# Kernel optimization log

Hardware: AMD Instinct MI355X
Metric: run time of the kernel (lower is better)

The kernel has to match this reference:

```python
import jax, jax.numpy as jnp
import numpy as np

L = 2          # num_layers
B = 32         # batch
T = 64         # max_sequence_length (= source len here)
H = 1024       # hidden_size
E = 1024       # embedding_size (== H so layer weights stack uniformly)
V = 16000      # vocab (in == out)


def _cell(x, h, c, Wih, Whh, bih, bhh):
    # PyTorch LSTM gate order: i, f, g, o
    g = x @ Wih.T + h @ Whh.T + (bih + bhh)
    i, f, gg, o = jnp.split(g, 4, axis=-1)
    c_new = jax.nn.sigmoid(f) * c + jax.nn.sigmoid(i) * jnp.tanh(gg)
    h_new = jax.nn.sigmoid(o) * jnp.tanh(c_new)
    return h_new, c_new


def _stack_step(h, c, x, Wih, Whh, bih, bhh):
    # h, c: (L, B, H); x: (B, E). Fixed small loop over layers.
    hs, cs, inp = [], [], x
    for l in range(L):
        nh, nc = _cell(inp, h[l], c[l], Wih[l], Whh[l], bih[l], bhh[l])
        hs.append(nh); cs.append(nc); inp = nh
    return jnp.stack(hs), jnp.stack(cs), inp


def setup_inputs() -> dict:
    key = jax.random.key(0)
    ks = jax.random.split(key, 16)
    s = 1.0 / np.sqrt(H)
    U = lambda k, shp: jax.random.uniform(k, shp, jnp.float32, -s, s)
    inp = {
        "input_ids": jax.random.randint(ks[0], (B, T), 0, V),
        "output_ids": jax.random.randint(ks[1], (B, T), 0, V),
        "enc_emb": jax.random.normal(ks[2], (V, E), jnp.float32),
        "enc_Wih": U(ks[3], (L, 4 * H, H)),
        "enc_Whh": U(ks[4], (L, 4 * H, H)),
        "enc_bih": U(ks[5], (L, 4 * H)),
        "enc_bhh": U(ks[6], (L, 4 * H)),
        "dec_emb": jax.random.normal(ks[7], (V, E), jnp.float32),
        "dec_Wih": U(ks[8], (L, 4 * H, H)),
        "dec_Whh": U(ks[9], (L, 4 * H, H)),
        "dec_bih": U(ks[10], (L, 4 * H)),
        "dec_bhh": U(ks[11], (L, 4 * H)),
        "Wout": U(ks[12], (V, H)),
        "bout": U(ks[13], (V,)),
    }
    return inp


def reference(input_ids, output_ids, enc_emb, enc_Wih, enc_Whh, enc_bih, enc_bhh,
              dec_emb, dec_Wih, dec_Whh, dec_bih, dec_bhh, Wout, bout):
    dtype = enc_emb.dtype
    # ---- Encoder: run LSTM over source, keep final (h, c) ----
    enc_x = enc_emb[input_ids]                      # (B, T, E); dropout is identity (eval)
    h0 = jnp.zeros((L, B, H), dtype)
    c0 = jnp.zeros((L, B, H), dtype)

    def enc_step(carry, xt):
        h, c = carry
        h, c, _ = _stack_step(h, c, xt, enc_Wih, enc_Whh, enc_bih, enc_bhh)
        return (h, c), None

    (h, c), _ = jax.lax.scan(enc_step, (h0, c0), jnp.swapaxes(enc_x, 0, 1))

    # ---- Decoder: teacher-forced; step i consumes output_ids[:, i-1] ----
    dec_x = dec_emb[output_ids[:, : T - 1]]         # (B, T-1, E)

    def dec_step(carry, xt):
        h, c = carry
        h, c, top = _stack_step(h, c, xt, dec_Wih, dec_Whh, dec_bih, dec_bhh)
        logit = top @ Wout.T + bout                  # (B, V)
        return (h, c), logit

    (_, _), logits_seq = jax.lax.scan(dec_step, (h, c), jnp.swapaxes(dec_x, 0, 1))

    # ---- Assemble logits like the torch code ----
    logits = jnp.zeros((B, T, V), dtype)
    # torch: logits[:, 0, output_ids[:, 0]] = 1  (broadcasts over both batch dims)
    logits = logits.at[:, 0, output_ids[:, 0]].set(1.0)
    logits = logits.at[:, 1:, :].set(jnp.swapaxes(logits_seq, 0, 1))
    return logits
```

## Files before the change

### kernel.cpp

```cpp
#include <hip/hip_runtime.h>

namespace {

constexpr int kB = 32;
constexpr int kT = 64;
constexpr int kH = 1024;
constexpr int kE = 1024;
constexpr int kV = 16000;
constexpr int kG = 4096;

typedef __attribute__((ext_vector_type(8))) short short8v;
typedef __attribute__((ext_vector_type(4))) float f32x4;

__device__ __forceinline__ float sigmoid_f(float x) {
  return 1.0f / (1.0f + __expf(-x));
}
__device__ __forceinline__ unsigned short f2bf(float x) {
  unsigned int u = __builtin_bit_cast(unsigned int, x);
  u = (u + 0x7FFFu + ((u >> 16) & 1u)) >> 16;
  return (unsigned short)u;
}
__device__ __forceinline__ float bf2f(unsigned short h) {
  return __builtin_bit_cast(float, (unsigned int)h << 16);
}

__global__ void zero_t0_kernel(float* __restrict__ out) {
  int idx = blockIdx.x * blockDim.x + threadIdx.x;
  if (idx >= kB * kV) return;
  int b = idx / kV, v = idx % kV;
  __builtin_nontemporal_store(0.0f, &out[(size_t)b * kT * kV + v]);
}

__global__ void ones_t0_kernel(const int* __restrict__ output_ids,
                               float* __restrict__ out) {
  int b = threadIdx.x >> 5;
  int j = threadIdx.x & 31;
  int id = output_ids[j * kT];
  out[(size_t)b * kT * kV + id] = 1.0f;
}

__global__ __launch_bounds__(256)
void convert_frag(const float* __restrict__ src, unsigned short* __restrict__ dst,
                  int nchunks) {
  const int idx = blockIdx.x * 256 + threadIdx.x;
  if (idx >= nchunks) return;
  const int lane = idx & 63;
  const int s = (idx >> 6) & 31;
  const int rg = idx >> 11;
  const int row = rg * 16 + (lane & 15);
  const int k = s * 32 + ((lane >> 4) << 3);
  const float4* p = reinterpret_cast<const float4*>(src + (size_t)row * kH + k);
  float4 v0 = p[0], v1 = p[1];
  short8v o;
  o[0] = (short)f2bf(v0.x); o[1] = (short)f2bf(v0.y);
  o[2] = (short)f2bf(v0.z); o[3] = (short)f2bf(v0.w);
  o[4] = (short)f2bf(v1.x); o[5] = (short)f2bf(v1.y);
  o[6] = (short)f2bf(v1.z); o[7] = (short)f2bf(v1.w);
  *reinterpret_cast<short8v*>(dst + (size_t)idx * 8) = o;
}

__global__ __launch_bounds__(256)
void convert_cell(const float* __restrict__ src, unsigned short* __restrict__ dst,
                  int nchunks) {
  const int idx = blockIdx.x * 256 + threadIdx.x;
  if (idx >= nchunks) return;
  const int l = idx & 63;
  const int kstep = (idx >> 6) & 31;
  const int uq = (idx >> 11) & 1;
  const int ub = idx >> 12;
  const int n = l & 15;
  const int row = (n >> 2) * kH + ub * 8 + uq * 4 + (n & 3);
  const int k = kstep * 32 + ((l >> 4) << 3);
  const float4* p = reinterpret_cast<const float4*>(src + (size_t)row * kH + k);
  float4 v0 = p[0], v1 = p[1];
  short8v o;
  o[0] = (short)f2bf(v0.x); o[1] = (short)f2bf(v0.y);
  o[2] = (short)f2bf(v0.z); o[3] = (short)f2bf(v0.w);
  o[4] = (short)f2bf(v1.x); o[5] = (short)f2bf(v1.y);
  o[6] = (short)f2bf(v1.z); o[7] = (short)f2bf(v1.w);
  *reinterpret_cast<short8v*>(dst + (size_t)idx * 8) = o;
}

__global__ __launch_bounds__(256)
void gather_frag(const float* __restrict__ emb, const int* __restrict__ ids,
                 unsigned short* __restrict__ dst, int ntiles) {
  const int idx = blockIdx.x * 256 + threadIdx.x;
  const int lane = idx & 63;
  const int s = (idx >> 6) & 31;
  const int tile = idx >> 11;
  if (tile >= ntiles) return;
  const int m = tile * 16 + (lane & 15);
  const int t = m >> 5, b = m & 31;
  const int id = ids[b * kT + t];
  const int k = s * 32 + ((lane >> 4) << 3);
  const float4* p = reinterpret_cast<const float4*>(emb + (size_t)id * kE + k);
  float4 v0 = p[0], v1 = p[1];
  short8v o;
  o[0] = (short)f2bf(v0.x); o[1] = (short)f2bf(v0.y);
  o[2] = (short)f2bf(v0.z); o[3] = (short)f2bf(v0.w);
  o[4] = (short)f2bf(v1.x); o[5] = (short)f2bf(v1.y);
  o[6] = (short)f2bf(v1.z); o[7] = (short)f2bf(v1.w);
  *reinterpret_cast<short8v*>(dst + (size_t)idx * 8) = o;
}

__global__ __launch_bounds__(256)
void proj_mfma(const unsigned short* __restrict__ Af,
               const unsigned short* __restrict__ Bf,
               const float* __restrict__ b0, const float* __restrict__ b1,
               unsigned short* __restrict__ dst, int nmt) {
  const int w = threadIdx.x >> 6, lane = threadIdx.x & 63;
  const int mg = blockIdx.x, ng = blockIdx.y;
  f32x4 acc[4][2] = {};
  const unsigned short* Ab[4];
  const unsigned short* Bb[2];
#pragma unroll
  for (int i = 0; i < 4; ++i) {
    int tile = mg * 4 + i;
    if (tile > nmt - 1) tile = nmt - 1;
    Ab[i] = Af + (size_t)tile * 16384 + lane * 8;
  }
#pragma unroll
  for (int j = 0; j < 2; ++j) {
    const int nt = ng * 8 + w * 2 + j;
    Bb[j] = Bf + (size_t)nt * 16384 + lane * 8;
  }
#pragma unroll 2
  for (int s = 0; s < 32; ++s) {
    short8v a[4], b[2];
#pragma unroll
    for (int i = 0; i < 4; ++i) a[i] = *reinterpret_cast<const short8v*>(Ab[i] + s * 512);
#pragma unroll
    for (int j = 0; j < 2; ++j) b[j] = *reinterpret_cast<const short8v*>(Bb[j] + s * 512);
#pragma unroll
    for (int i = 0; i < 4; ++i)
#pragma unroll
      for (int j = 0; j < 2; ++j)
        acc[i][j] = __builtin_amdgcn_mfma_f32_16x16x32_bf16(a[i], b[j], acc[i][j], 0, 0, 0);
  }
#pragma unroll
  for (int i = 0; i < 4; ++i) {
    const int tile = mg * 4 + i;
    if (tile >= nmt) continue;
    const int mbase = tile * 16 + ((lane >> 4) << 2);
#pragma unroll
    for (int j = 0; j < 2; ++j) {
      const int n = (ng * 8 + w * 2 + j) * 16 + (lane & 15);
      const float bj = b0[n] + b1[n];
      const int g = n >> 10;
      const int u = n & 1023;
      const int q = u >> 2;
      const int uu = u & 3;
#pragma unroll
      for (int r = 0; r < 4; ++r) {
        const int m2 = mbase + r;
        const int t = m2 >> 5, mb = m2 & 31;
        dst[(size_t)t * kB * kG + (size_t)(q * 32 + mb) * 16 + g * 4 + uu] =
            f2bf(acc[i][j][r] + bj);
      }
    }
  }
}

__global__ __launch_bounds__(256)
void out_gemm_mfma(const unsigned short* __restrict__ Af,
                   const unsigned short* __restrict__ Bf,
                   const float* __restrict__ bias, float* __restrict__ out) {
  const int w = threadIdx.x >> 6, lane = threadIdx.x & 63;
  const int mg = blockIdx.x, ng = blockIdx.y;
  __shared__ float LsF[64 * 260];
  f32x4 acc[4][4] = {};
  const unsigned short* Ab[4];
  const unsigned short* Bb[4];
#pragma unroll
  for (int i = 0; i < 4; ++i) {
    int tile = mg * 4 + i;
    if (tile > 125) tile = 125;
    Ab[i] = Af + (size_t)tile * 16384 + lane * 8;
  }
#pragma unroll
  for (int j = 0; j < 4; ++j) {
    int nt = ng * 16 + w * 4 + j;
    if (nt > 999) nt = 999;
    Bb[j] = Bf + (size_t)nt * 16384 + lane * 8;
  }
#pragma unroll 2
  for (int s = 0; s < 32; ++s) {
    short8v a[4], b[4];
#pragma unroll
    for (int i = 0; i < 4; ++i) a[i] = *reinterpret_cast<const short8v*>(Ab[i] + s * 512);
#pragma unroll
    for (int j = 0; j < 4; ++j) b[j] = *reinterpret_cast<const short8v*>(Bb[j] + s * 512);
#pragma unroll
    for (int i = 0; i < 4; ++i)
#pragma unroll
      for (int j = 0; j < 4; ++j)
        acc[i][j] = __builtin_amdgcn_mfma_f32_16x16x32_bf16(a[i], b[j], acc[i][j], 0, 0, 0);
  }
#pragma unroll
  for (int i = 0; i < 4; ++i) {
    const int r2b = i * 16 + ((lane >> 4) << 2);
#pragma unroll
    for (int j = 0; j < 4; ++j) {
      const int nloc = (w * 4 + j) * 16 + (lane & 15);
#pragma unroll
      for (int r = 0; r < 4; ++r) LsF[(r2b + r) * 260 + nloc] = acc[i][j][r];
    }
  }
  __syncthreads();
  const int nglob = ng * 256 + lane * 4;
  if (nglob >= kV) return;
  const f32x4 b4 = *reinterpret_cast<const f32x4*>(&bias[nglob]);
#pragma unroll
  for (int it = 0; it < 16; ++it) {
    const int r2 = w * 16 + it;
    const int m = mg * 64 + r2;
    if (m >= 2016) break;
    f32x4 v = *reinterpret_cast<const f32x4*>(&LsF[r2 * 260 + lane * 4]);
    v += b4;
    const int sd = m >> 5, bb = m & 31;
    f32x4* dst = reinterpret_cast<f32x4*>(
        &out[(size_t)bb * kT * kV + (size_t)(sd + 1) * kV + nglob]);
    __builtin_nontemporal_store(v, dst);
  }
}

struct CellJob {
  const unsigned short* A0;
  const unsigned short* A1;
  const unsigned short* Wih1;
  const unsigned short* Whh1;
  const unsigned short* Whh0;
  const unsigned short* xprojc;
  const float* bih1;
  const float* bhh1;
  float* c0;
  float* c1;
  unsigned short* h0_out;
  unsigned short* h1_out;
  unsigned short* htop_out;
  int has_l0, has_l1;
};

__global__ __launch_bounds__(512)
void lstm_pair(CellJob J) {
  const int q = blockIdx.x;
  const int tid = threadIdx.x;
  const int wave = tid >> 6;
  const int lane = tid & 63;
  __shared__ alignas(16) float Ls[3][8][2][64][4];

  f32x4 aI0 = {0.f, 0.f, 0.f, 0.f}, aI1 = {0.f, 0.f, 0.f, 0.f};
  f32x4 aJ0 = {0.f, 0.f, 0.f, 0.f}, aJ1 = {0.f, 0.f, 0.f, 0.f};
  f32x4 aH0 = {0.f, 0.f, 0.f, 0.f}, aH1 = {0.f, 0.f, 0.f, 0.f};
  const int ksb = wave * 4;
#pragma unroll
  for (int s = 0; s < 4; ++s) {
    const int ks = ksb + s;
    const size_t widx = ((size_t)(q * 32 + ks) * 64 + lane) * 8;
    const short8v a00 =
        *reinterpret_cast<const short8v*>(J.A0 + (size_t)(ks * 64 + lane) * 8);
    const short8v a01 =
        *reinterpret_cast<const short8v*>(J.A0 + (size_t)((32 + ks) * 64 + lane) * 8);
    if (J.has_l1) {
      const short8v bi = *reinterpret_cast<const short8v*>(J.Wih1 + widx);
      aI0 = __builtin_amdgcn_mfma_f32_16x16x32_bf16(a00, bi, aI0, 0, 0, 0);
      aI1 = __builtin_amdgcn_mfma_f32_16x16x32_bf16(a01, bi, aI1, 0, 0, 0);
      const short8v a10 =
          *reinterpret_cast<const short8v*>(J.A1 + (size_t)(ks * 64 + lane) * 8);
      const short8v a11 =
          *reinterpret_cast<const short8v*>(J.A1 + (size_t)((32 + ks) * 64 + lane) * 8);
      const short8v bh1 = *reinterpret_cast<const short8v*>(J.Whh1 + widx);
      aJ0 = __builtin_amdgcn_mfma_f32_16x16x32_bf16(a10, bh1, aJ0, 0, 0, 0);
      aJ1 = __builtin_amdgcn_mfma_f32_16x16x32_bf16(a11, bh1, aJ1, 0, 0, 0);
    }
    if (J.has_l0) {
      const short8v bh0 = *reinterpret_cast<const short8v*>(J.Whh0 + widx);
      aH0 = __builtin_amdgcn_mfma_f32_16x16x32_bf16(a00, bh0, aH0, 0, 0, 0);
      aH1 = __builtin_amdgcn_mfma_f32_16x16x32_bf16(a01, bh0, aH1, 0, 0, 0);
    }
  }
  *reinterpret_cast<f32x4*>(&Ls[0][wave][0][lane][0]) = aI0;
  *reinterpret_cast<f32x4*>(&Ls[0][wave][1][lane][0]) = aI1;
  *reinterpret_cast<f32x4*>(&Ls[1][wave][0][lane][0]) = aJ0;
  *reinterpret_cast<f32x4*>(&Ls[1][wave][1][lane][0]) = aJ1;
  *reinterpret_cast<f32x4*>(&Ls[2][wave][0][lane][0]) = aH0;
  *reinterpret_cast<f32x4*>(&Ls[2][wave][1][lane][0]) = aH1;
  __syncthreads();

  if (tid < 128) {
    const int m = tid >> 2;
    const int ul = tid & 3;
    const int u = q * 4 + ul;
    const int mt = m >> 4, r = m & 3;
    const int lm = (m & 12) << 2;
    const int ksu = u >> 5;
    const int lane3 = (m & 15) | (((u >> 3) & 3) << 4);
    const int e = u & 7;
    const size_t fidx = (size_t)((mt * 32 + ksu) * 64 + lane3) * 8 + e;

    if (J.has_l0) {
      float g0[4];
#pragma unroll
      for (int g = 0; g < 4; ++g) {
        const int ln = (g * 4 + ul) | lm;
        float v = 0.f;
#pragma unroll
        for (int ww = 0; ww < 8; ++ww) v += Ls[2][ww][mt][ln][r];
        v += bf2f(J.xprojc[(q * 32 + m) * 16 + g * 4 + ul]);
        g0[g] = v;
      }
      const float cold = J.c0[m * kH + u];
      const float cnew = sigmoid_f(g0[1]) * cold + sigmoid_f(g0[0]) * tanhf(g0[2]);
      const float hnew = sigmoid_f(g0[3]) * tanhf(cnew);
      J.c0[m * kH + u] = cnew;
      J.h0_out[fidx] = f2bf(hnew);
    }
    if (J.has_l1) {
      float g1[4];
#pragma unroll
      for (int g = 0; g < 4; ++g) {
        const int ln = (g * 4 + ul) | lm;
        float v = 0.f;
#pragma unroll
        for (int ww = 0; ww < 8; ++ww)
          v += Ls[0][ww][mt][ln][r] + Ls[1][ww][mt][ln][r];
        v += J.bih1[g * kH + u] + J.bhh1[g * kH + u];
        g1[g] = v;
      }
      const float cold = J.c1[m * kH + u];
      const float cnew = sigmoid_f(g1[1]) * cold + sigmoid_f(g1[0]) * tanhf(g1[2]);
      const float hnew = sigmoid_f(g1[3]) * tanhf(cnew);
      J.c1[m * kH + u] = cnew;
      const unsigned short hb = f2bf(hnew);
      J.h1_out[fidx] = hb;
      if (J.htop_out) J.htop_out[fidx] = hb;
    }
  }
}

}

extern "C" void kernel_launch(void* const* d_in, const int* in_sizes, int n_in,
                              void* d_out, int out_size, void* d_ws, size_t ws_size,
                              hipStream_t stream) {
  const int* input_ids = (const int*)d_in[0];
  const int* output_ids = (const int*)d_in[1];
  const float* enc_emb = (const float*)d_in[2];
  const float* enc_Wih = (const float*)d_in[3];
  const float* enc_Whh = (const float*)d_in[4];
  const float* enc_bih = (const float*)d_in[5];
  const float* enc_bhh = (const float*)d_in[6];
  const float* dec_emb = (const float*)d_in[7];
  const float* dec_Wih = (const float*)d_in[8];
  const float* dec_Whh = (const float*)d_in[9];
  const float* dec_bih = (const float*)d_in[10];
  const float* dec_bhh = (const float*)d_in[11];
  const float* Wout = (const float*)d_in[12];
  const float* bout = (const float*)d_in[13];
  float* out = (float*)d_out;
  char* ws = (char*)d_ws;

  const size_t WL = (size_t)kG * kH;

  size_t off = 0;
  unsigned short* wout_frag = (unsigned short*)(ws + 0);
  unsigned short* xproj_enc = (unsigned short*)(ws + off); off += (size_t)kT * kB * kG * 2;
  unsigned short* xin_enc = (unsigned short*)(ws + off); off += (size_t)kT * kB * kH * 2;
  unsigned short* wih0_enc = (unsigned short*)(ws + off); off += WL * 2;
  unsigned short* wih0_dec = (unsigned short*)(ws + off); off += WL * 2;
  unsigned short* xproj_dec = (unsigned short*)(ws + off); off += (size_t)(kT - 1) * kB * kG * 2;
  unsigned short* xin_dec = (unsigned short*)(ws + off); off += (size_t)(kT - 1) * kB * kH * 2;
  unsigned short* htop_frag = xin_dec;
  float* c0 = (float*)(ws + off); off += (size_t)kB * kH * 4;
  float* c1 = (float*)(ws + off); off += (size_t)kB * kH * 4;
  unsigned short* h0swz[2];
  unsigned short* h1swz[2];
  h0swz[0] = (unsigned short*)(ws + off); off += (size_t)kB * kH * 2;
  h0swz[1] = (unsigned short*)(ws + off); off += (size_t)kB * kH * 2;
  h1swz[0] = (unsigned short*)(ws + off); off += (size_t)kB * kH * 2;
  h1swz[1] = (unsigned short*)(ws + off); off += (size_t)kB * kH * 2;
  unsigned short* wswz[6];
  for (int i = 0; i < 6; ++i) { wswz[i] = (unsigned short*)(ws + off); off += WL * 2; }

  (void)hipMemsetAsync(c0, 0, (size_t)kB * kH * (4 + 4 + 2 + 2 + 2 + 2), stream);

  const int wchunks = kG * (kH / 8);
  convert_cell<<<2048, 256, 0, stream>>>(enc_Whh, wswz[0], wchunks);
  convert_cell<<<2048, 256, 0, stream>>>(enc_Wih + WL, wswz[1], wchunks);
  convert_cell<<<2048, 256, 0, stream>>>(enc_Whh + WL, wswz[2], wchunks);
  convert_cell<<<2048, 256, 0, stream>>>(dec_Whh, wswz[3], wchunks);
  convert_cell<<<2048, 256, 0, stream>>>(dec_Wih + WL, wswz[4], wchunks);
  convert_cell<<<2048, 256, 0, stream>>>(dec_Whh + WL, wswz[5], wchunks);
  convert_frag<<<2048, 256, 0, stream>>>(enc_Wih, wih0_enc, wchunks);
  convert_frag<<<2048, 256, 0, stream>>>(dec_Wih, wih0_dec, wchunks);

  gather_frag<<<128 * 8, 256, 0, stream>>>(enc_emb, input_ids, xin_enc, 128);
  gather_frag<<<126 * 8, 256, 0, stream>>>(dec_emb, output_ids, xin_dec, 126);

  proj_mfma<<<dim3(32, 32), 256, 0, stream>>>(xin_enc, wih0_enc, enc_bih, enc_bhh,
                                              xproj_enc, 128);
  proj_mfma<<<dim3(32, 32), 256, 0, stream>>>(xin_dec, wih0_dec, dec_bih, dec_bhh,
                                              xproj_dec, 126);

  for (int p = 0; p <= 127; ++p) {
    CellJob J = {};
    J.has_l0 = (p <= 126);
    J.has_l1 = (p >= 1);
    J.A0 = h0swz[p & 1];
    J.A1 = h1swz[(p + 1) & 1];
    J.c0 = c0;
    J.c1 = c1;
    if (J.has_l0) {
      J.Whh0 = (p < kT) ? wswz[0] : wswz[3];
      J.xprojc = (p < kT) ? (xproj_enc + (size_t)p * kB * kG)
                          : (xproj_dec + (size_t)(p - kT) * kB * kG);
      J.h0_out = h0swz[(p + 1) & 1];
    } else {
      J.Whh0 = wswz[3];
      J.xprojc = xproj_dec;
      J.h0_out = h0swz[(p + 1) & 1];
    }
    if (J.has_l1) {
      const bool e1 = (p - 1) < kT;
      J.Wih1 = e1 ? wswz[1] : wswz[4];
      J.Whh1 = e1 ? wswz[2] : wswz[5];
      J.bih1 = (e1 ? enc_bih : dec_bih) + kG;
      J.bhh1 = (e1 ? enc_bhh : dec_bhh) + kG;
      J.h1_out = h1swz[p & 1];
      J.htop_out = (p - 1 >= kT) ? (htop_frag + (size_t)(p - 1 - kT) * kB * kH)
                                 : nullptr;
    } else {
      J.Wih1 = wswz[1];
      J.Whh1 = wswz[2];
      J.bih1 = enc_bih + kG;
      J.bhh1 = enc_bhh + kG;
      J.h1_out = h1swz[p & 1];
      J.htop_out = nullptr;
    }
    lstm_pair<<<256, 512, 0, stream>>>(J);
    if (p == 63) {
      convert_frag<<<8000, 256, 0, stream>>>(Wout, wout_frag, kV * (kH / 8));
    }
  }

  zero_t0_kernel<<<(kB * kV + 255) / 256, 256, 0, stream>>>(out);
  ones_t0_kernel<<<1, kB * kB, 0, stream>>>(output_ids, out);

  out_gemm_mfma<<<dim3(32, 63), 256, 0, stream>>>(htop_frag, wout_frag, bout, out);
}
```

Before: 1.174 ms.

## Process two gate tiles per LSTM block and swizzle output GEMM blocks

The recurrent lstm_pair kernel now has each block compute two unit groups, so each loaded activation fragment is reused across twice as many weight tiles, and the grid drops from 256 to 128 blocks. The layer guards around the MFMA loop are removed, so both layers' products are always computed. The output GEMM maps a 1D grid through an XCD-style swizzle for better L2 locality, and it writes its epilogue through a half-sized LDS buffer in two phases to lower shared-memory use. The trade-off is that the per-step recurrent kernel now uses only half as many CUs, which may hurt a latency-bound step.

```diff
diff --git a/kernel.cpp b/kernel.cpp
--- a/kernel.cpp
+++ b/kernel.cpp
@@ -166,8 +166,10 @@
                    const unsigned short* __restrict__ Bf,
                    const float* __restrict__ bias, float* __restrict__ out) {
   const int w = threadIdx.x >> 6, lane = threadIdx.x & 63;
-  const int mg = blockIdx.x, ng = blockIdx.y;
-  __shared__ float LsF[64 * 260];
+  const int bid = blockIdx.x;
+  const int swz = (bid & 7) * 252 + (bid >> 3);
+  const int mg = swz & 31, ng = swz >> 5;
+  __shared__ float LsF[32 * 260];
   f32x4 acc[4][4] = {};
   const unsigned short* Ab[4];
   const unsigned short* Bb[4];
@@ -196,31 +198,38 @@
       for (int j = 0; j < 4; ++j)
         acc[i][j] = __builtin_amdgcn_mfma_f32_16x16x32_bf16(a[i], b[j], acc[i][j], 0, 0, 0);
   }
-#pragma unroll
-  for (int i = 0; i < 4; ++i) {
-    const int r2b = i * 16 + ((lane >> 4) << 2);
-#pragma unroll
-    for (int j = 0; j < 4; ++j) {
-      const int nloc = (w * 4 + j) * 16 + (lane & 15);
-#pragma unroll
-      for (int r = 0; r < 4; ++r) LsF[(r2b + r) * 260 + nloc] = acc[i][j][r];
-    }
-  }
-  __syncthreads();
   const int nglob = ng * 256 + lane * 4;
-  if (nglob >= kV) return;
-  const f32x4 b4 = *reinterpret_cast<const f32x4*>(&bias[nglob]);
-#pragma unroll
-  for (int it = 0; it < 16; ++it) {
-    const int r2 = w * 16 + it;
-    const int m = mg * 64 + r2;
-    if (m >= 2016) break;
-    f32x4 v = *reinterpret_cast<const f32x4*>(&LsF[r2 * 260 + lane * 4]);
-    v += b4;
-    const int sd = m >> 5, bb = m & 31;
-    f32x4* dst = reinterpret_cast<f32x4*>(
-        &out[(size_t)bb * kT * kV + (size_t)(sd + 1) * kV + nglob]);
-    __builtin_nontemporal_store(v, dst);
+  f32x4 b4 = {0.f, 0.f, 0.f, 0.f};
+  if (nglob < kV) b4 = *reinterpret_cast<const f32x4*>(&bias[nglob]);
+#pragma unroll
+  for (int ph = 0; ph < 2; ++ph) {
+    if (ph) __syncthreads();
+#pragma unroll
+    for (int i2 = 0; i2 < 2; ++i2) {
+      const int i = ph * 2 + i2;
+      const int r2b = i2 * 16 + ((lane >> 4) << 2);
+#pragma unroll
+      for (int j = 0; j < 4; ++j) {
+        const int nloc = (w * 4 + j) * 16 + (lane & 15);
+#pragma unroll
+        for (int r = 0; r < 4; ++r) LsF[(r2b + r) * 260 + nloc] = acc[i][j][r];
+      }
+    }
+    __syncthreads();
+    if (nglob < kV) {
+#pragma unroll
+      for (int it = 0; it < 8; ++it) {
+        const int r2l = w * 8 + it;
+        const int m = mg * 64 + ph * 32 + r2l;
+        if (m >= 2016) break;
+        f32x4 v = *reinterpret_cast<const f32x4*>(&LsF[r2l * 260 + lane * 4]);
+        v += b4;
+        const int sd = m >> 5, bb = m & 31;
+        f32x4* dst = reinterpret_cast<f32x4*>(
+            &out[(size_t)bb * kT * kV + (size_t)(sd + 1) * kV + nglob]);
+        __builtin_nontemporal_store(v, dst);
+      }
+    }
   }
 }
 
@@ -243,53 +252,58 @@
 
 __global__ __launch_bounds__(512)
 void lstm_pair(CellJob J) {
-  const int q = blockIdx.x;
+  const int blk = blockIdx.x;
   const int tid = threadIdx.x;
   const int wave = tid >> 6;
   const int lane = tid & 63;
-  __shared__ alignas(16) float Ls[3][8][2][64][4];
-
-  f32x4 aI0 = {0.f, 0.f, 0.f, 0.f}, aI1 = {0.f, 0.f, 0.f, 0.f};
-  f32x4 aJ0 = {0.f, 0.f, 0.f, 0.f}, aJ1 = {0.f, 0.f, 0.f, 0.f};
-  f32x4 aH0 = {0.f, 0.f, 0.f, 0.f}, aH1 = {0.f, 0.f, 0.f, 0.f};
+  __shared__ alignas(16) float Ls[2][3][8][2][64][4];
+
+  f32x4 aI[2][2] = {};
+  f32x4 aJ[2][2] = {};
+  f32x4 aH[2][2] = {};
   const int ksb = wave * 4;
 #pragma unroll
   for (int s = 0; s < 4; ++s) {
     const int ks = ksb + s;
-    const size_t widx = ((size_t)(q * 32 + ks) * 64 + lane) * 8;
     const short8v a00 =
         *reinterpret_cast<const short8v*>(J.A0 + (size_t)(ks * 64 + lane) * 8);
     const short8v a01 =
         *reinterpret_cast<const short8v*>(J.A0 + (size_t)((32 + ks) * 64 + lane) * 8);
-    if (J.has_l1) {
+    const short8v a10 =
+        *reinterpret_cast<const short8v*>(J.A1 + (size_t)(ks * 64 + lane) * 8);
+    const short8v a11 =
+        *reinterpret_cast<const short8v*>(J.A1 + (size_t)((32 + ks) * 64 + lane) * 8);
+#pragma unroll
+    for (int qq = 0; qq < 2; ++qq) {
+      const int q = blk * 2 + qq;
+      const size_t widx = ((size_t)(q * 32 + ks) * 64 + lane) * 8;
       const short8v bi = *reinterpret_cast<const short8v*>(J.Wih1 + widx);
-      aI0 = __builtin_amdgcn_mfma_f32_16x16x32_bf16(a00, bi, aI0, 0, 0, 0);
-      aI1 = __builtin_amdgcn_mfma_f32_16x16x32_bf16(a01, bi, aI1, 0, 0, 0);
-      const short8v a10 =
-          *reinterpret_cast<const short8v*>(J.A1 + (size_t)(ks * 64 + lane) * 8);
-      const short8v a11 =
-          *reinterpret_cast<const short8v*>(J.A1 + (size_t)((32 + ks) * 64 + lane) * 8);
+      aI[qq][0] = __builtin_amdgcn_mfma_f32_16x16x32_bf16(a00, bi, aI[qq][0], 0, 0, 0);
+      aI[qq][1] = __builtin_amdgcn_mfma_f32_16x16x32_bf16(a01, bi, aI[qq][1], 0, 0, 0);
       const short8v bh1 = *reinterpret_cast<const short8v*>(J.Whh1 + widx);
-      aJ0 = __builtin_amdgcn_mfma_f32_16x16x32_bf16(a10, bh1, aJ0, 0, 0, 0);
-      aJ1 = __builtin_amdgcn_mfma_f32_16x16x32_bf16(a11, bh1, aJ1, 0, 0, 0);
-    }
-    if (J.has_l0) {
+      aJ[qq][0] = __builtin_amdgcn_mfma_f32_16x16x32_bf16(a10, bh1, aJ[qq][0], 0, 0, 0);
+      aJ[qq][1] = __builtin_amdgcn_mfma_f32_16x16x32_bf16(a11, bh1, aJ[qq][1], 0, 0, 0);
       const short8v bh0 = *reinterpret_cast<const short8v*>(J.Whh0 + widx);
-      aH0 = __builtin_amdgcn_mfma_f32_16x16x32_bf16(a00, bh0, aH0, 0, 0, 0);
-      aH1 = __builtin_amdgcn_mfma_f32_16x16x32_bf16(a01, bh0, aH1, 0, 0, 0);
-    }
-  }
-  *reinterpret_cast<f32x4*>(&Ls[0][wave][0][lane][0]) = aI0;
-  *reinterpret_cast<f32x4*>(&Ls[0][wave][1][lane][0]) = aI1;
-  *reinterpret_cast<f32x4*>(&Ls[1][wave][0][lane][0]) = aJ0;
-  *reinterpret_cast<f32x4*>(&Ls[1][wave][1][lane][0]) = aJ1;
-  *reinterpret_cast<f32x4*>(&Ls[2][wave][0][lane][0]) = aH0;
-  *reinterpret_cast<f32x4*>(&Ls[2][wave][1][lane][0]) = aH1;
+      aH[qq][0] = __builtin_amdgcn_mfma_f32_16x16x32_bf16(a00, bh0, aH[qq][0], 0, 0, 0);
+      aH[qq][1] = __builtin_amdgcn_mfma_f32_16x16x32_bf16(a01, bh0, aH[qq][1], 0, 0, 0);
+    }
+  }
+#pragma unroll
+  for (int qq = 0; qq < 2; ++qq) {
+#pragma unroll
+    for (int mt = 0; mt < 2; ++mt) {
+      *reinterpret_cast<f32x4*>(&Ls[qq][0][wave][mt][lane][0]) = aI[qq][mt];
+      *reinterpret_cast<f32x4*>(&Ls[qq][1][wave][mt][lane][0]) = aJ[qq][mt];
+      *reinterpret_cast<f32x4*>(&Ls[qq][2][wave][mt][lane][0]) = aH[qq][mt];
+    }
+  }
   __syncthreads();
 
-  if (tid < 128) {
-    const int m = tid >> 2;
+  if (tid < 256) {
+    const int qq = tid >> 7;
+    const int m = (tid >> 2) & 31;
     const int ul = tid & 3;
+    const int q = blk * 2 + qq;
     const int u = q * 4 + ul;
     const int mt = m >> 4, r = m & 3;
     const int lm = (m & 12) << 2;
@@ -305,7 +319,7 @@
         const int ln = (g * 4 + ul) | lm;
         float v = 0.f;
 #pragma unroll
-        for (int ww = 0; ww < 8; ++ww) v += Ls[2][ww][mt][ln][r];
+        for (int ww = 0; ww < 8; ++ww) v += Ls[qq][2][ww][mt][ln][r];
         v += bf2f(J.xprojc[(q * 32 + m) * 16 + g * 4 + ul]);
         g0[g] = v;
       }
@@ -323,7 +337,7 @@
         float v = 0.f;
 #pragma unroll
         for (int ww = 0; ww < 8; ++ww)
-          v += Ls[0][ww][mt][ln][r] + Ls[1][ww][mt][ln][r];
+          v += Ls[qq][0][ww][mt][ln][r] + Ls[qq][1][ww][mt][ln][r];
         v += J.bih1[g * kH + u] + J.bhh1[g * kH + u];
         g1[g] = v;
       }
@@ -437,7 +451,7 @@
       J.h1_out = h1swz[p & 1];
       J.htop_out = nullptr;
     }
-    lstm_pair<<<256, 512, 0, stream>>>(J);
+    lstm_pair<<<128, 512, 0, stream>>>(J);
     if (p == 63) {
       convert_frag<<<8000, 256, 0, stream>>>(Wout, wout_frag, kV * (kH / 8));
     }
@@ -446,5 +460,5 @@
   zero_t0_kernel<<<(kB * kV + 255) / 256, 256, 0, stream>>>(out);
   ones_t0_kernel<<<1, kB * kB, 0, stream>>>(output_ids, out);
 
-  out_gemm_mfma<<<dim3(32, 63), 256, 0, stream>>>(htop_frag, wout_frag, bout, out);
-}
+  out_gemm_mfma<<<2016, 256, 0, stream>>>(htop_frag, wout_frag, bout, out);
+}
```

New measurement: 1.576 ms. 1.34x slower.
